# Performance work log

Hardware: AMD Instinct MI355X
Metric: run time of the kernel (lower is better)

Reference implementation:

```python
import jax, jax.numpy as jnp
import numpy as np

T = 0.07          # cfg.CAP.TEMP
K = 50            # cfg.CAP.HARD_NEG_K
LOSS_WEIGHT = 0.5 # cfg.CAP.LOSS_WEIGHT
C_CAM = 8         # number of cameras
P = 2048          # pseudo-ID classes per camera bank


def setup_inputs() -> dict:
    key = jax.random.key(0)
    k1, k2, k3, k4 = jax.random.split(key, 4)
    B, D = 256, 2048
    inputs = jax.random.normal(k1, (B, D), jnp.float32)
    labels = jax.random.randint(k2, (B,), 0, P)
    cams = jax.random.randint(k3, (B,), 0, C_CAM)
    tempV = jax.random.normal(k4, (C_CAM * P, D), jnp.float32)
    tempV = tempV / jnp.linalg.norm(tempV, axis=1, keepdims=True)  # memory rows are L2-normalized
    return {"inputs": inputs, "labels": labels, "cams": cams, "tempV": tempV}


def _seg_mean_sum(vals, cams):
    # original loops over unique cams: loss += mean(vals within cam); empty cams contribute 0
    sums = jax.ops.segment_sum(vals, cams, num_segments=C_CAM)
    cnts = jax.ops.segment_sum(jnp.ones_like(vals), cams, num_segments=C_CAM)
    return jnp.sum(jnp.where(cnts > 0, sums / jnp.maximum(cnts, 1.0), 0.0))


def reference(inputs, labels, cams, tempV):
    B = inputs.shape[0]
    # cfg.CAP.NORM_FEAT
    x = inputs / jnp.linalg.norm(inputs, axis=1, keepdims=True)

    # one fused matmul against the concatenated memory; per-camera banks are contiguous P-slices
    all_logits = x @ tempV.T                      # [B, C_CAM*P]
    logits3 = all_logits.reshape(B, C_CAM, P)

    # ---- intra-camera loss: logits against the sample's own camera bank ----
    percam = jnp.take_along_axis(logits3, cams[:, None, None], axis=1)[:, 0, :] / T  # [B, P]
    lse_i = jax.scipy.special.logsumexp(percam, axis=1)
    ce = lse_i - jnp.take_along_axis(percam, labels[:, None], axis=1)[:, 0]
    loss_intra = _seg_mean_sum(ce, cams)

    # ---- inter-camera loss with hard-negative mining ----
    rows = jnp.arange(B)[:, None]
    # each ID has one centroid in every camera bank: positions label + P*cam
    ori_ind = labels[:, None] + P * jnp.arange(C_CAM)[None, :]        # [B, C_CAM]
    sims = all_logits.at[rows, ori_ind].set(-10000.0)                 # mask positives
    _, sel_ind = jax.lax.top_k(sims, K)                               # hard negatives (== sort[-K:])
    ori_logits = jnp.take_along_axis(all_logits, ori_ind, axis=1) / T  # [B, C_CAM]
    sel_logits = jnp.take_along_axis(all_logits, sel_ind, axis=1) / T  # [B, K]
    cat = jnp.concatenate([ori_logits, sel_logits], axis=1)            # [B, C_CAM+K]
    lse_c = jax.scipy.special.logsumexp(cat, axis=1)
    # target = 1/len(ori) on positives, 0 on negatives -> lse - mean(positive logits)
    loss_k = lse_c - jnp.mean(ori_logits, axis=1)
    loss_inter = LOSS_WEIGHT * _seg_mean_sum(loss_k, cams)

    return (loss_intra, loss_inter)
```

## Files before the change

kernel.cpp:

```cpp
#include <hip/hip_runtime.h>
#include <hip/hip_bf16.h>

#define BATCH 256
#define DIM   2048
#define NMEM  16384
#define PCLS  2048
#define CCAM  8
#define KSEL  50
#define T_INV 14.285714285714285714f
#define NBIN  4096

typedef __bf16 bf16x8 __attribute__((ext_vector_type(8)));
typedef float  f32x4  __attribute__((ext_vector_type(4)));

#define AS_GLOBAL __attribute__((address_space(1)))
#define AS_LDS    __attribute__((address_space(3)))

static __device__ __forceinline__ unsigned int f2bf(float f) {
  unsigned int u = __float_as_uint(f);
  return (u + 0x7FFFu + ((u >> 16) & 1u)) >> 16;
}
static __device__ __forceinline__ unsigned int pk2(float lo, float hi) {
  return f2bf(lo) | (f2bf(hi) << 16);
}
static __device__ __forceinline__ int binof(float v) {
  float bf = fmaf(v, 1950.4762f, 2048.0f);
  bf = fminf(fmaxf(bf, 0.0f), 4095.0f);
  return (int)bf;
}

__global__ __launch_bounds__(256) void norm_cast_kernel(
    const float* __restrict__ in, unsigned short* __restrict__ xb) {
  __shared__ float red[256];
  const int b = blockIdx.x, t = threadIdx.x;
  const float4* row = (const float4*)(in + (size_t)b * DIM);
  float4 a0 = row[t];
  float4 a1 = row[t + 256];
  float ss = a0.x*a0.x + a0.y*a0.y + a0.z*a0.z + a0.w*a0.w
           + a1.x*a1.x + a1.y*a1.y + a1.z*a1.z + a1.w*a1.w;
  red[t] = ss; __syncthreads();
  for (int s = 128; s > 0; s >>= 1) { if (t < s) red[t] += red[t + s]; __syncthreads(); }
  const float rn = rsqrtf(red[0]);
  ushort4 o0, o1;
  o0.x = (unsigned short)f2bf(a0.x*rn); o0.y = (unsigned short)f2bf(a0.y*rn);
  o0.z = (unsigned short)f2bf(a0.z*rn); o0.w = (unsigned short)f2bf(a0.w*rn);
  o1.x = (unsigned short)f2bf(a1.x*rn); o1.y = (unsigned short)f2bf(a1.y*rn);
  o1.z = (unsigned short)f2bf(a1.z*rn); o1.w = (unsigned short)f2bf(a1.w*rn);
  *(ushort4*)&xb[(size_t)b * DIM + t * 4]         = o0;
  *(ushort4*)&xb[(size_t)b * DIM + (t + 256) * 4] = o1;
}

#define BM 128
#define BN 64
#define BK 64
#define KHALF (DIM / 2)
#define NTH   (KHALF / BK)

__global__ __launch_bounds__(256, 4) void gemm_kernel(
    const unsigned short* __restrict__ X,
    const float* __restrict__ V,
    float* __restrict__ C) {
  __shared__ __align__(16) unsigned short As[BM * BK];
  __shared__ __align__(16) float          Bs[BN * BK];
  const int t  = threadIdx.x;
  const int m0 = blockIdx.x * BM;
  const int n0 = blockIdx.y * BN;
  const int kb = blockIdx.z * KHALF;
  const int lane = t & 63;
  const int w    = t >> 6;
  const int wm   = (w >> 1) * 64;
  const int wn   = (w & 1) * 32;
  const int fr   = lane & 15;
  const int fko  = lane >> 4;

  f32x4 acc[4][2];
#pragma unroll
  for (int i = 0; i < 4; i++)
#pragma unroll
    for (int j = 0; j < 2; j++) acc[i][j] = (f32x4){0.f, 0.f, 0.f, 0.f};

  const unsigned short* Abase =
      X + (size_t)(m0 + w * 32 + (lane >> 3)) * DIM + kb
        + ((lane & 7) ^ (lane >> 3)) * 8;
  const float* Bbase = V + (size_t)(n0 + w * 16 + (lane >> 4)) * DIM + kb;
  const int cB = (lane & 15) ^ (lane >> 4);

  for (int kt = 0; kt < NTH; kt++) {
    const int k0 = kt * BK;
#pragma unroll
    for (int q = 0; q < 4; q++) {
      __builtin_amdgcn_global_load_lds(
          (const AS_GLOBAL unsigned int*)(Abase + (size_t)q * 8 * DIM + k0),
          (AS_LDS unsigned int*)&As[(w * 32 + q * 8) * BK],
          16, 0, 0);
    }
#pragma unroll
    for (int q = 0; q < 4; q++) {
      const int c = cB ^ (q * 4);
      __builtin_amdgcn_global_load_lds(
          (const AS_GLOBAL unsigned int*)(Bbase + (size_t)q * 4 * DIM + k0 + c * 4),
          (AS_LDS unsigned int*)&Bs[(w * 16 + q * 4) * BK],
          16, 0, 0);
    }
    __syncthreads();

#pragma unroll
    for (int kk = 0; kk < BK; kk += 32) {
      bf16x8 aF[4], bF[2];
#pragma unroll
      for (int i = 0; i < 4; i++) {
        const int R  = wm + i * 16 + fr;
        const int c0 = (kk >> 3) + fko;
        const int p  = c0 ^ (fr & 7);
        aF[i] = *(const bf16x8*)&As[R * BK + p * 8];
      }
#pragma unroll
      for (int j = 0; j < 2; j++) {
        const int RN = wn + j * 16 + fr;
        const int c0 = (kk + fko * 8) >> 2;
        const int p0 = c0 ^ fr, p1 = (c0 + 1) ^ fr;
        const float4* Brow = (const float4*)&Bs[RN * BK];
        const float4 lo = Brow[p0];
        const float4 hi = Brow[p1];
        uint4 pk;
        pk.x = pk2(lo.x, lo.y); pk.y = pk2(lo.z, lo.w);
        pk.z = pk2(hi.x, hi.y); pk.w = pk2(hi.z, hi.w);
        bF[j] = *(bf16x8*)&pk;
      }
#pragma unroll
      for (int i = 0; i < 4; i++)
#pragma unroll
        for (int j = 0; j < 2; j++)
          acc[i][j] = __builtin_amdgcn_mfma_f32_16x16x32_bf16(aF[i], bF[j], acc[i][j], 0, 0, 0);
    }
    __syncthreads();
  }

  const int cr = (lane >> 4) * 4;
  const int cc = lane & 15;
#pragma unroll
  for (int i = 0; i < 4; i++)
#pragma unroll
    for (int j = 0; j < 2; j++)
#pragma unroll
      for (int r = 0; r < 4; r++)
        unsafeAtomicAdd(
            &C[(size_t)(m0 + wm + i * 16 + cr + r) * NMEM + (n0 + wn + j * 16 + cc)],
            acc[i][j][r]);
}

__global__ __launch_bounds__(256) void row_loss_kernel(
    const float* __restrict__ logits,
    const int* __restrict__ labels, const int* __restrict__ cams,
    float* __restrict__ ce_out, float* __restrict__ lossk_out) {
  __shared__ float vals[NMEM];
  __shared__ int   hist[NBIN];
  __shared__ float red[256];
  __shared__ int   pint[256];
  __shared__ float bl[512];
  __shared__ int   bcount;
  __shared__ int   bstar_s, cabove_s;

  const int b = blockIdx.x, t = threadIdx.x;
  const float4* src = (const float4*)(logits + (size_t)b * NMEM);
#pragma unroll
  for (int i = 0; i < 16; i++) ((float4*)vals)[t + 256 * i] = src[t + 256 * i];
#pragma unroll
  for (int i = 0; i < NBIN / 256; i++) hist[t + 256 * i] = 0;
  if (t == 0) bcount = 0;
  const int cam = cams[b], label = labels[b];
  __syncthreads();

  const int s0 = cam * PCLS;
  float S = 0.f;
#pragma unroll
  for (int i = 0; i < 8; i++) S += __expf(vals[s0 + t + 256 * i] * T_INV);
  red[t] = S; __syncthreads();
  for (int s = 128; s > 0; s >>= 1) { if (t < s) red[t] += red[t + s]; __syncthreads(); }
  float ov[CCAM]; float sumo = 0.f;
  if (t == 0) {
    ce_out[b] = logf(red[0]) - vals[s0 + label] * T_INV;
#pragma unroll
    for (int c = 0; c < CCAM; c++) { ov[c] = vals[c * PCLS + label]; sumo += ov[c]; }
  }
  __syncthreads();
  if (t < CCAM) vals[t * PCLS + label] = -1e30f;
  __syncthreads();

#pragma unroll
  for (int i = 0; i < 64; i++) {
    int bin = binof(vals[t + 256 * i]);
    atomicAdd(&hist[bin], 1);
  }
  __syncthreads();

  int ps = 0;
#pragma unroll
  for (int i = 0; i < 16; i++) ps += hist[t * 16 + i];
  pint[t] = ps; __syncthreads();
  if (t == 0) {
    int cum = 0, bstar = 0, cab = 0;
    for (int tc = 255; tc >= 0; tc--) {
      if (cum + pint[tc] >= KSEL) {
        for (int bi = tc * 16 + 15; bi >= tc * 16; bi--) {
          int h = hist[bi];
          if (cum + h >= KSEL) { bstar = bi; cab = cum; break; }
          cum += h;
        }
        break;
      }
      cum += pint[tc];
    }
    bstar_s = bstar; cabove_s = cab;
  }
  __syncthreads();
  const int bstar = bstar_s;

  float S2 = 0.f;
#pragma unroll
  for (int i = 0; i < 64; i++) {
    float v = vals[t + 256 * i];
    int bin = binof(v);
    if (bin > bstar) S2 += __expf(v * T_INV);
    else if (bin == bstar) {
      int p = atomicAdd(&bcount, 1);
      if (p < 512) bl[p] = v;
    }
  }
  red[t] = S2; __syncthreads();
  for (int s = 128; s > 0; s >>= 1) { if (t < s) red[t] += red[t + s]; __syncthreads(); }

  if (t == 0) {
    float S2tot = red[0];
    int need = KSEL - cabove_s;
    int bc = min(bcount, 512);
    for (int r = 0; r < need; r++) {
      float mx = -1e30f; int mi = 0;
      for (int i = 0; i < bc; i++) if (bl[i] > mx) { mx = bl[i]; mi = i; }
      S2tot += __expf(mx * T_INV);
      bl[mi] = -1e30f;
    }
#pragma unroll
    for (int c = 0; c < CCAM; c++) S2tot += __expf(ov[c] * T_INV);
    lossk_out[b] = logf(S2tot) - (sumo * T_INV) * (1.0f / CCAM);
  }
}

__global__ __launch_bounds__(256) void finalize_kernel(
    const float* __restrict__ ce, const float* __restrict__ lossk,
    const int* __restrict__ cams, float* __restrict__ out) {
  __shared__ float ce_s[BATCH], lk_s[BATCH];
  __shared__ int   cam_s[BATCH];
  __shared__ float si[CCAM], sk[CCAM], cnt[CCAM];
  const int t = threadIdx.x;
  ce_s[t]  = ce[t];
  lk_s[t]  = lossk[t];
  cam_s[t] = cams[t];
  __syncthreads();
  if (t < CCAM) {
    float a = 0.f, b = 0.f; int n = 0;
    for (int i = 0; i < BATCH; i++) {
      if (cam_s[i] == t) { a += ce_s[i]; b += lk_s[i]; n++; }
    }
    si[t] = a; sk[t] = b; cnt[t] = (float)n;
  }
  __syncthreads();
  if (t == 0) {
    float li = 0.f, lk = 0.f;
    for (int c = 0; c < CCAM; c++) {
      if (cnt[c] > 0.f) { li += si[c] / cnt[c]; lk += sk[c] / cnt[c]; }
    }
    out[0] = li;
    out[1] = 0.5f * lk;
  }
}

extern "C" void kernel_launch(void* const* d_in, const int* in_sizes, int n_in,
                              void* d_out, int out_size, void* d_ws, size_t ws_size,
                              hipStream_t stream) {
  const float* inputs = (const float*)d_in[0];
  const int*   labels = (const int*)d_in[1];
  const int*   cams   = (const int*)d_in[2];
  const float* tempV  = (const float*)d_in[3];
  float* out = (float*)d_out;

  char* ws = (char*)d_ws;
  unsigned short* xb  = (unsigned short*)ws;
  float* logits       = (float*)(ws + (1u << 20));
  float* ce           = (float*)(ws + (1u << 20) + (16u << 20));
  float* lossk        = (float*)(ws + (1u << 20) + (16u << 20) + 1024);

  norm_cast_kernel<<<BATCH, 256, 0, stream>>>(inputs, xb);
  hipMemsetAsync(logits, 0, (size_t)BATCH * NMEM * sizeof(float), stream);
  gemm_kernel<<<dim3(BATCH / BM, NMEM / BN, 2), 256, 0, stream>>>(xb, tempV, logits);
  row_loss_kernel<<<BATCH, 256, 0, stream>>>(logits, labels, cams, ce, lossk);
  finalize_kernel<<<1, 256, 0, stream>>>(ce, lossk, cams, out);
}
```

Baseline: 275.3 us.

## Cover full batch per GEMM block and triple-buffer K tiles with async LDS loads

The GEMM block tile now spans all 256 batch rows with 512 threads, so each fp32 memory row of tempV is fetched once instead of once per M block. The K step shrinks to 32. A three-stage LDS ring is prefetched with global_load_lds, using explicit vmcnt waits and a single barrier per iteration in place of the two full syncthreads. The intent is to halve the dominant tempV traffic and overlap loads with MFMA work. The costs are larger blocks, more LDS per block and fewer blocks in the grid.

```diff
diff --git a/kernel.cpp b/kernel.cpp
--- a/kernel.cpp
+++ b/kernel.cpp
@@ -15,6 +15,9 @@
 
 #define AS_GLOBAL __attribute__((address_space(1)))
 #define AS_LDS    __attribute__((address_space(3)))
+
+#define WAITCNT_VM3 0xF73
+#define WAITCNT_VM0 0xF70
 
 static __device__ __forceinline__ unsigned int f2bf(float f) {
   unsigned int u = __float_as_uint(f);
@@ -50,20 +53,19 @@
   *(ushort4*)&xb[(size_t)b * DIM + (t + 256) * 4] = o1;
 }
 
-#define BM 128
+#define BM 256
 #define BN 64
-#define BK 64
+#define BK 32
 #define KHALF (DIM / 2)
-#define NTH   (KHALF / BK)
-
-__global__ __launch_bounds__(256, 4) void gemm_kernel(
+#define NT    (KHALF / BK)
+
+__global__ __launch_bounds__(512, 4) void gemm_kernel(
     const unsigned short* __restrict__ X,
     const float* __restrict__ V,
     float* __restrict__ C) {
-  __shared__ __align__(16) unsigned short As[BM * BK];
-  __shared__ __align__(16) float          Bs[BN * BK];
+  __shared__ __align__(16) unsigned short As[3][BM * BK];
+  __shared__ __align__(16) float          Bs[3][BN * BK];
   const int t  = threadIdx.x;
-  const int m0 = blockIdx.x * BM;
   const int n0 = blockIdx.y * BN;
   const int kb = blockIdx.z * KHALF;
   const int lane = t & 63;
@@ -79,61 +81,69 @@
 #pragma unroll
     for (int j = 0; j < 2; j++) acc[i][j] = (f32x4){0.f, 0.f, 0.f, 0.f};
 
-  const unsigned short* Abase =
-      X + (size_t)(m0 + w * 32 + (lane >> 3)) * DIM + kb
-        + ((lane & 7) ^ (lane >> 3)) * 8;
-  const float* Bbase = V + (size_t)(n0 + w * 16 + (lane >> 4)) * DIM + kb;
-  const int cB = (lane & 15) ^ (lane >> 4);
-
-  for (int kt = 0; kt < NTH; kt++) {
-    const int k0 = kt * BK;
-#pragma unroll
-    for (int q = 0; q < 4; q++) {
+  const unsigned short* Xp =
+      X + (size_t)(w * 32 + (lane >> 2)) * DIM + kb
+        + (((lane & 3) ^ ((lane >> 2) & 3)) * 8);
+  const float* Vp =
+      V + (size_t)(n0 + w * 8 + (lane >> 3)) * DIM + kb
+        + (((lane & 7) ^ ((lane >> 3) & 7)) * 4);
+
+  auto glds_tile = [&](int buf, int k0) {
+#pragma unroll
+    for (int q = 0; q < 2; q++) {
       __builtin_amdgcn_global_load_lds(
-          (const AS_GLOBAL unsigned int*)(Abase + (size_t)q * 8 * DIM + k0),
-          (AS_LDS unsigned int*)&As[(w * 32 + q * 8) * BK],
+          (const AS_GLOBAL unsigned int*)(Xp + (size_t)q * 16 * DIM + k0),
+          (AS_LDS unsigned int*)&As[buf][(w * 32 + q * 16) * BK],
           16, 0, 0);
     }
-#pragma unroll
-    for (int q = 0; q < 4; q++) {
-      const int c = cB ^ (q * 4);
-      __builtin_amdgcn_global_load_lds(
-          (const AS_GLOBAL unsigned int*)(Bbase + (size_t)q * 4 * DIM + k0 + c * 4),
-          (AS_LDS unsigned int*)&Bs[(w * 16 + q * 4) * BK],
-          16, 0, 0);
-    }
-    __syncthreads();
-
-#pragma unroll
-    for (int kk = 0; kk < BK; kk += 32) {
-      bf16x8 aF[4], bF[2];
-#pragma unroll
-      for (int i = 0; i < 4; i++) {
-        const int R  = wm + i * 16 + fr;
-        const int c0 = (kk >> 3) + fko;
-        const int p  = c0 ^ (fr & 7);
-        aF[i] = *(const bf16x8*)&As[R * BK + p * 8];
-      }
-#pragma unroll
-      for (int j = 0; j < 2; j++) {
-        const int RN = wn + j * 16 + fr;
-        const int c0 = (kk + fko * 8) >> 2;
-        const int p0 = c0 ^ fr, p1 = (c0 + 1) ^ fr;
-        const float4* Brow = (const float4*)&Bs[RN * BK];
-        const float4 lo = Brow[p0];
-        const float4 hi = Brow[p1];
-        uint4 pk;
-        pk.x = pk2(lo.x, lo.y); pk.y = pk2(lo.z, lo.w);
-        pk.z = pk2(hi.x, hi.y); pk.w = pk2(hi.z, hi.w);
-        bF[j] = *(bf16x8*)&pk;
-      }
-#pragma unroll
-      for (int i = 0; i < 4; i++)
-#pragma unroll
-        for (int j = 0; j < 2; j++)
-          acc[i][j] = __builtin_amdgcn_mfma_f32_16x16x32_bf16(aF[i], bF[j], acc[i][j], 0, 0, 0);
-    }
-    __syncthreads();
+    __builtin_amdgcn_global_load_lds(
+        (const AS_GLOBAL unsigned int*)(Vp + k0),
+        (AS_LDS unsigned int*)&Bs[buf][(w * 8) * BK],
+        16, 0, 0);
+  };
+
+  auto compute = [&](int buf) {
+    bf16x8 aF[4], bF[2];
+    const int pa = fko ^ (fr & 3);
+#pragma unroll
+    for (int i = 0; i < 4; i++) {
+      const int R = wm + i * 16 + fr;
+      aF[i] = *(const bf16x8*)&As[buf][R * BK + pa * 8];
+    }
+    const int p0 = (2 * fko) ^ (fr & 7);
+#pragma unroll
+    for (int j = 0; j < 2; j++) {
+      const int RN = wn + j * 16 + fr;
+      const float4* Brow = (const float4*)&Bs[buf][RN * BK];
+      const float4 lo = Brow[p0];
+      const float4 hi = Brow[p0 ^ 1];
+      uint4 pk;
+      pk.x = pk2(lo.x, lo.y); pk.y = pk2(lo.z, lo.w);
+      pk.z = pk2(hi.x, hi.y); pk.w = pk2(hi.z, hi.w);
+      bF[j] = *(bf16x8*)&pk;
+    }
+#pragma unroll
+    for (int i = 0; i < 4; i++)
+#pragma unroll
+      for (int j = 0; j < 2; j++)
+        acc[i][j] = __builtin_amdgcn_mfma_f32_16x16x32_bf16(aF[i], bF[j], acc[i][j], 0, 0, 0);
+  };
+
+  glds_tile(0, 0);
+
+  int cur = 0;
+  for (int kt = 0; kt < NT; kt++) {
+    if (kt + 1 < NT) {
+      int nxt = cur + 1; if (nxt == 3) nxt = 0;
+      glds_tile(nxt, (kt + 1) * BK);
+      __builtin_amdgcn_s_waitcnt(WAITCNT_VM3);
+    } else {
+      __builtin_amdgcn_s_waitcnt(WAITCNT_VM0);
+    }
+    __builtin_amdgcn_s_barrier();
+    __builtin_amdgcn_sched_barrier(0);
+    compute(cur);
+    cur = cur + 1; if (cur == 3) cur = 0;
   }
 
   const int cr = (lane >> 4) * 4;
@@ -145,7 +155,7 @@
 #pragma unroll
       for (int r = 0; r < 4; r++)
         unsafeAtomicAdd(
-            &C[(size_t)(m0 + wm + i * 16 + cr + r) * NMEM + (n0 + wn + j * 16 + cc)],
+            &C[(size_t)(wm + i * 16 + cr + r) * NMEM + (n0 + wn + j * 16 + cc)],
             acc[i][j][r]);
 }
 
@@ -292,7 +302,7 @@
 
   norm_cast_kernel<<<BATCH, 256, 0, stream>>>(inputs, xb);
   hipMemsetAsync(logits, 0, (size_t)BATCH * NMEM * sizeof(float), stream);
-  gemm_kernel<<<dim3(BATCH / BM, NMEM / BN, 2), 256, 0, stream>>>(xb, tempV, logits);
+  gemm_kernel<<<dim3(1, NMEM / BN, 2), 512, 0, stream>>>(xb, tempV, logits);
   row_loss_kernel<<<BATCH, 256, 0, stream>>>(logits, labels, cams, ce, lossk);
   finalize_kernel<<<1, 256, 0, stream>>>(ce, lossk, cams, out);
 }
```

Measured after the change: 287.2 us. 1.04x slower.
